# Kernel tuning notes

Measured on AMD Instinct MI355X. Metric: run time of the kernel, lower is better.

## Reference

```python
import jax, jax.numpy as jnp
import numpy as np

LATENT_DIM = 32
NB_LABEL = 10
B = 4096


def _conv4(x, w, b):
    # stride-4 kernel-4 conv == non-overlapping 4x4 patch contraction
    Bn, C, H, W = x.shape
    xp = x.reshape(Bn, C, H // 4, 4, W // 4, 4)
    return jnp.einsum('bcipjq,ocpq->boij', xp, w) + b[None, :, None, None]


def _deconv4(x, w, b):
    # stride-4 kernel-4 ConvTranspose2d, padding 0: each pixel expands to a 4x4 block
    Bn, C, H, W = x.shape
    y = jnp.einsum('bcij,copq->boipjq', x, w)  # w: (Cin, Cout, 4, 4)
    return y.reshape(Bn, w.shape[1], H * 4, W * 4) + b[None, :, None, None]


def setup_inputs() -> dict:
    key = jax.random.key(0)
    ks = jax.random.split(key, 24)
    s = 0.05

    def rn(k, shape, scale=s):
        return jax.random.normal(k, shape, dtype=jnp.float32) * scale

    return {
        'x': jax.random.normal(ks[0], (B, 1, 64, 64), dtype=jnp.float32),
        'z': jax.random.normal(ks[1], (B, NB_LABEL), dtype=jnp.float32),
        'u_in': jax.random.normal(ks[2], (B, 2), dtype=jnp.float32),
        'conv1_w': rn(ks[3], (16, 1, 4, 4)), 'conv1_b': rn(ks[4], (16,)),
        'conv2_w': rn(ks[5], (64, 16, 4, 4)), 'conv2_b': rn(ks[6], (64,)),
        'conv3_w': rn(ks[7], (256, 64, 4, 4)), 'conv3_b': rn(ks[8], (256,)),
        'w_xz': rn(ks[9], (32, 256)),
        'w_label': rn(ks[10], (NB_LABEL, 32)),
        'w_zd1': rn(ks[11], (LATENT_DIM, NB_LABEL)),
        'w_zd2': rn(ks[12], (LATENT_DIM, NB_LABEL)),
        'w_xu': rn(ks[13], (32, 256)),
        'w_mu': rn(ks[14], (2, 32)),
        'w_logvar': rn(ks[15], (2, 32)),
        'tc_w': rn(ks[16], (LATENT_DIM, 256, 2)),
        'tc_b': rn(ks[17], (LATENT_DIM, 256)),
        'dec3_w': rn(ks[18], (256, 64, 4, 4)), 'dec3_b': rn(ks[19], (64,)),
        'dec2_w': rn(ks[20], (64, 16, 4, 4)), 'dec2_b': rn(ks[21], (16,)),
        'dec1_w': rn(ks[22], (16, 1, 4, 4)), 'dec1_b': jnp.zeros((1,), dtype=jnp.float32),
    }


def reference(x, z, u_in, conv1_w, conv1_b, conv2_w, conv2_b, conv3_w, conv3_b,
              w_xz, w_label, w_zd1, w_zd2, w_xu, w_mu, w_logvar, tc_w, tc_b,
              dec3_w, dec3_b, dec2_w, dec2_b, dec1_w, dec1_b):
    h = jax.nn.relu(_conv4(x, conv1_w, conv1_b))
    h = jax.nn.relu(_conv4(h, conv2_w, conv2_b))
    h = jax.nn.relu(_conv4(h, conv3_w, conv3_b))
    h = h.reshape(h.shape[0], -1)                       # (B, 256)

    x_z = jax.nn.relu(h @ w_xz.T)                       # (B, 32)
    z_logit = x_z @ w_label.T                           # (B, 10)

    key = jax.random.key(42)
    k_cat, k_eps = jax.random.split(key)
    z_hat = jax.random.categorical(k_cat, z_logit, axis=-1)       # (B,)
    z_onehot = jax.nn.one_hot(z_hat, NB_LABEL, dtype=z_logit.dtype)
    z_d1 = z_onehot @ w_zd1.T                           # (B, 32)
    z_d2 = z_onehot @ w_zd2.T                           # (B, 32)

    x_u = jax.nn.relu(h @ w_xu.T)                       # (B, 32)
    mu = x_u @ w_mu.T                                   # (B, 2)
    logvar = x_u @ w_logvar.T                           # (B, 2)
    std = jnp.exp(0.5 * logvar)
    eps = jax.random.normal(k_eps, std.shape, dtype=std.dtype)
    u_out = eps * std + mu                              # (B, 2)

    # all 32 tiny Linear(2->256)+ReLU collapsed into one batched einsum
    trans = u_out[:, None, :] + jnp.stack([z_d1, z_d2], axis=-1)   # (B, 32, 2)
    x_hat = jax.nn.relu(jnp.einsum('bic,ioc->bio', trans, tc_w) + tc_b[None]).sum(axis=1)  # (B, 256)
    transfo_d1 = trans[:, :, 0]                         # (B, 32)
    transfo_d2 = trans[:, :, 1]

    d = x_hat.reshape(-1, 256, 1, 1)
    d = jax.nn.relu(_deconv4(d, dec3_w, dec3_b))        # (B, 64, 4, 4)
    d = jax.nn.relu(_deconv4(d, dec2_w, dec2_b))        # (B, 16, 16, 16)
    x_hat_logit = _deconv4(d, dec1_w, dec1_b)           # (B, 1, 64, 64)

    return (z_logit, z_hat.reshape(-1, 1), mu, logvar, u_out, x_hat_logit, transfo_d1, transfo_d2)
```

## Files before the change

### kernel.cpp

```cpp
#include <hip/hip_runtime.h>
#include <stdint.h>

#define B_TOT 4096

#define OFF_ZL 0
#define OFF_ZH 40960
#define OFF_MU 45056
#define OFF_LV 53248
#define OFF_UO 61440
#define OFF_XL 69632
#define OFF_T1 16846848
#define OFF_T2 16977920

typedef __attribute__((ext_vector_type(8))) short bf16x8;
typedef __attribute__((ext_vector_type(4))) float f32x4;

__device__ __forceinline__ unsigned short f2b(float f) {
  unsigned int u = __float_as_uint(f);
  return (unsigned short)((u + 0x7FFFu + ((u >> 16) & 1u)) >> 16);
}
__device__ __forceinline__ float b2f(unsigned short b) {
  return __uint_as_float(((unsigned int)b) << 16);
}

#define TF_ROUND(r) do { x0 += x1; x1 = (x1 << (r)) | (x1 >> (32-(r))); x1 ^= x0; } while(0)

__device__ __forceinline__ void threefry(uint32_t k0, uint32_t k1,
                                         uint32_t c0, uint32_t c1,
                                         uint32_t& o0, uint32_t& o1) {
  uint32_t ks2 = k0 ^ k1 ^ 0x1BD11BDAu;
  uint32_t x0 = c0 + k0, x1 = c1 + k1;
  TF_ROUND(13); TF_ROUND(15); TF_ROUND(26); TF_ROUND(6);
  x0 += k1;  x1 += ks2 + 1u;
  TF_ROUND(17); TF_ROUND(29); TF_ROUND(16); TF_ROUND(24);
  x0 += ks2; x1 += k0 + 2u;
  TF_ROUND(13); TF_ROUND(15); TF_ROUND(26); TF_ROUND(6);
  x0 += k0;  x1 += k1 + 3u;
  TF_ROUND(17); TF_ROUND(29); TF_ROUND(16); TF_ROUND(24);
  x0 += k1;  x1 += ks2 + 4u;
  TF_ROUND(13); TF_ROUND(15); TF_ROUND(26); TF_ROUND(6);
  x0 += ks2; x1 += k0 + 5u;
  o0 = x0; o1 = x1;
}

__device__ __forceinline__ uint32_t tf_bits32(uint32_t k0, uint32_t k1, uint32_t j) {
  uint32_t r0, r1;
  threefry(k0, k1, 0u, j, r0, r1);
  return r0 ^ r1;
}

__device__ __forceinline__ float erfinv_xla(float x) {
  float w = -log1pf(-x * x);
  float p;
  if (w < 5.0f) {
    w -= 2.5f;
    p = 2.81022636e-08f;
    p = fmaf(p, w, 3.43273939e-07f);
    p = fmaf(p, w, -3.5233877e-06f);
    p = fmaf(p, w, -4.39150654e-06f);
    p = fmaf(p, w, 0.00021858087f);
    p = fmaf(p, w, -0.00125372503f);
    p = fmaf(p, w, -0.00417768164f);
    p = fmaf(p, w, 0.246640727f);
    p = fmaf(p, w, 1.50140941f);
  } else {
    w = sqrtf(w) - 3.0f;
    p = -0.000200214257f;
    p = fmaf(p, w, 0.000100950558f);
    p = fmaf(p, w, 0.00134934322f);
    p = fmaf(p, w, -0.00367342844f);
    p = fmaf(p, w, 0.00573950773f);
    p = fmaf(p, w, -0.0076224613f);
    p = fmaf(p, w, 0.00943887047f);
    p = fmaf(p, w, 1.00167406f);
    p = fmaf(p, w, 2.83297682f);
  }
  return p * x;
}

__global__ __launch_bounds__(256) void k_prep(const float* __restrict__ w3,
    const float* __restrict__ w2, unsigned short* __restrict__ w3t,
    unsigned short* __restrict__ w2t) {
  int idx = blockIdx.x * 256 + threadIdx.x;
  unsigned short tmp[8];
  if (idx < 32768) {
    int np = idx >> 5, k0 = (idx & 31) * 8;
    int ic = np & 63, pos = np >> 6;
#pragma unroll
    for (int i = 0; i < 8; ++i)
      tmp[i] = f2b(w3[(size_t)(k0 + i) * 1024 + ic * 16 + pos]);
    *(bf16x8*)(w3t + (size_t)np * 256 + k0) = *(bf16x8*)tmp;
  } else if (idx < 32768 + 2048) {
    int j = idx - 32768;
    int n = j >> 3, k0 = (j & 7) * 8;
#pragma unroll
    for (int i = 0; i < 8; ++i)
      tmp[i] = f2b(w2[(size_t)(k0 + i) * 256 + n]);
    *(bf16x8*)(w2t + (size_t)n * 64 + k0) = *(bf16x8*)tmp;
  }
}

__global__ __launch_bounds__(256) void k_conv1(const float* __restrict__ x,
    const float* __restrict__ w, const float* __restrict__ bias,
    float* __restrict__ h1t) {
  __shared__ __align__(16) float ws[256];
  __shared__ float bs[16];
  int b = blockIdx.x, t = threadIdx.x;
  ws[t] = w[t];
  if (t < 16) bs[t] = bias[t];
  __syncthreads();
  int i = t >> 4, j = t & 15;
  const float* xb = x + (size_t)b * 4096;
  float4 xv[4];
#pragma unroll
  for (int p = 0; p < 4; ++p)
    xv[p] = *(const float4*)(xb + (4 * i + p) * 64 + 4 * j);
  float acc[16];
#pragma unroll
  for (int oc = 0; oc < 16; ++oc) acc[oc] = bs[oc];
#pragma unroll
  for (int p = 0; p < 4; ++p) {
    float4 xp = xv[p];
#pragma unroll
    for (int oc = 0; oc < 16; ++oc) {
      float4 wv = *(const float4*)(ws + oc * 16 + p * 4);
      acc[oc] = fmaf(xp.x, wv.x, acc[oc]);
      acc[oc] = fmaf(xp.y, wv.y, acc[oc]);
      acc[oc] = fmaf(xp.z, wv.z, acc[oc]);
      acc[oc] = fmaf(xp.w, wv.w, acc[oc]);
    }
  }
  float* hb = h1t + (size_t)b * 4096 + ((i >> 2) * 4 + (j >> 2)) * 256
            + (i & 3) * 4 + (j & 3);
#pragma unroll
  for (int oc = 0; oc < 16; ++oc)
    hb[oc * 16] = fmaxf(acc[oc], 0.0f);
}

__global__ __launch_bounds__(256) void k_conv2g(const float* __restrict__ A,
    const float* __restrict__ Bw, const float* __restrict__ bias,
    float* __restrict__ h2) {
  __shared__ __align__(16) float As[16][68];
  __shared__ __align__(16) float Bs[16][68];
  int t = threadIdx.x;
  int m0 = blockIdx.x * 64;
  int tx = t & 15, ty = t >> 4;
  float acc[4][4] = {};
  int lr = t >> 2, lk = (t & 3) * 4;
  for (int k0 = 0; k0 < 256; k0 += 16) {
    float4 a  = *(const float4*)(A  + (size_t)(m0 + lr) * 256 + k0 + lk);
    float4 bv = *(const float4*)(Bw + (size_t)lr * 256 + k0 + lk);
    As[lk + 0][lr] = a.x; As[lk + 1][lr] = a.y; As[lk + 2][lr] = a.z; As[lk + 3][lr] = a.w;
    Bs[lk + 0][lr] = bv.x; Bs[lk + 1][lr] = bv.y; Bs[lk + 2][lr] = bv.z; Bs[lk + 3][lr] = bv.w;
    __syncthreads();
#pragma unroll
    for (int kk = 0; kk < 16; ++kk) {
      float4 af = *(const float4*)(&As[kk][ty * 4]);
      float4 bf = *(const float4*)(&Bs[kk][tx * 4]);
      float av[4] = {af.x, af.y, af.z, af.w};
      float bb[4] = {bf.x, bf.y, bf.z, bf.w};
#pragma unroll
      for (int ii = 0; ii < 4; ++ii)
#pragma unroll
        for (int jj = 0; jj < 4; ++jj)
          acc[ii][jj] = fmaf(av[ii], bb[jj], acc[ii][jj]);
    }
    __syncthreads();
  }
  float4 bb4 = *(const float4*)(bias + tx * 4);
  float bb[4] = {bb4.x, bb4.y, bb4.z, bb4.w};
#pragma unroll
  for (int ii = 0; ii < 4; ++ii) {
    int row = m0 + ty * 4 + ii;
    int b = row >> 4, pos = row & 15;
    float* hp = h2 + (size_t)b * 1024 + pos;
#pragma unroll
    for (int jj = 0; jj < 4; ++jj)
      hp[(tx * 4 + jj) * 16] = fmaxf(acc[ii][jj] + bb[jj], 0.f);
  }
}

__global__ __launch_bounds__(256) void k_conv3p(const float* __restrict__ A,
    const float* __restrict__ w3, float* __restrict__ part) {
  __shared__ __align__(16) float As[16][68];
  __shared__ __align__(16) float Bs[16][68];
  int t = threadIdx.x;
  int m0 = blockIdx.x * 64, n0 = blockIdx.y * 64;
  int kb = blockIdx.z * 256;
  int tx = t & 15, ty = t >> 4;
  float acc[4][4] = {};
  int lr = t >> 2, lk = (t & 3) * 4;
  for (int k0 = kb; k0 < kb + 256; k0 += 16) {
    float4 a  = *(const float4*)(A  + (size_t)(m0 + lr) * 1024 + k0 + lk);
    float4 bv = *(const float4*)(w3 + (size_t)(n0 + lr) * 1024 + k0 + lk);
    As[lk + 0][lr] = a.x; As[lk + 1][lr] = a.y; As[lk + 2][lr] = a.z; As[lk + 3][lr] = a.w;
    Bs[lk + 0][lr] = bv.x; Bs[lk + 1][lr] = bv.y; Bs[lk + 2][lr] = bv.z; Bs[lk + 3][lr] = bv.w;
    __syncthreads();
#pragma unroll
    for (int kk = 0; kk < 16; ++kk) {
      float4 af = *(const float4*)(&As[kk][ty * 4]);
      float4 bf = *(const float4*)(&Bs[kk][tx * 4]);
      float av[4] = {af.x, af.y, af.z, af.w};
      float bb[4] = {bf.x, bf.y, bf.z, bf.w};
#pragma unroll
      for (int ii = 0; ii < 4; ++ii)
#pragma unroll
        for (int jj = 0; jj < 4; ++jj)
          acc[ii][jj] = fmaf(av[ii], bb[jj], acc[ii][jj]);
    }
    __syncthreads();
  }
  float* pc = part + (size_t)blockIdx.z * 1048576;
#pragma unroll
  for (int ii = 0; ii < 4; ++ii) {
    int row = m0 + ty * 4 + ii;
    *(float4*)(pc + (size_t)row * 256 + n0 + tx * 4) =
        make_float4(acc[ii][0], acc[ii][1], acc[ii][2], acc[ii][3]);
  }
}

__global__ __launch_bounds__(256) void k_c3red(const float* __restrict__ part,
    const float* __restrict__ b3, float* __restrict__ h) {
  int idx = blockIdx.x * 256 + threadIdx.x;
  int row = idx >> 6, c4 = (idx & 63) * 4;
  const float* p0 = part + (size_t)row * 256 + c4;
  float4 s  = *(const float4*)(p0);
  float4 s1 = *(const float4*)(p0 + 1048576);
  float4 s2 = *(const float4*)(p0 + 2097152);
  float4 s3 = *(const float4*)(p0 + 3145728);
  float4 bb = *(const float4*)(b3 + c4);
  float4 o;
  o.x = fmaxf(((s.x + s1.x) + s2.x) + s3.x + bb.x, 0.f);
  o.y = fmaxf(((s.y + s1.y) + s2.y) + s3.y + bb.y, 0.f);
  o.z = fmaxf(((s.z + s1.z) + s2.z) + s3.z + bb.z, 0.f);
  o.w = fmaxf(((s.w + s1.w) + s2.w) + s3.w + bb.w, 0.f);
  *(float4*)(h + (size_t)row * 256 + c4) = o;
}

__global__ __launch_bounds__(256) void k_dec3m(const unsigned short* __restrict__ xhb,
    const unsigned short* __restrict__ w3t, const float* __restrict__ bias,
    unsigned short* __restrict__ d3t) {
  int t = threadIdx.x;
  int lane = t & 63, wv = t >> 6;
  int m0 = blockIdx.x * 64, n0 = blockIdx.y * 64;
  int l15 = lane & 15, g8 = (lane >> 4) * 8;
  const unsigned short* arow = xhb + (size_t)(m0 + wv * 16 + l15) * 256 + g8;
  const unsigned short* brow = w3t + (size_t)(n0 + l15) * 256 + g8;
  f32x4 acc[4] = {};
  for (int kb = 0; kb < 256; kb += 32) {
    bf16x8 af = *(const bf16x8*)(arow + kb);
#pragma unroll
    for (int ns = 0; ns < 4; ++ns) {
      bf16x8 bf = *(const bf16x8*)(brow + (size_t)ns * 4096 + kb);
      acc[ns] = __builtin_amdgcn_mfma_f32_16x16x32_bf16(af, bf, acc[ns], 0, 0, 0);
    }
  }
  int rbase = (lane >> 4) * 4;
#pragma unroll
  for (int ns = 0; ns < 4; ++ns) {
    int ncol = n0 + ns * 16 + l15;
    float bb = bias[ncol & 63];
#pragma unroll
    for (int r = 0; r < 4; ++r) {
      float v = fmaxf(acc[ns][r] + bb, 0.f);
      d3t[(size_t)(m0 + wv * 16 + rbase + r) * 1024 + ncol] = f2b(v);
    }
  }
}

__global__ __launch_bounds__(256) void k_dec2m(const unsigned short* __restrict__ d3t,
    const unsigned short* __restrict__ w2t, const float* __restrict__ b2,
    const float* __restrict__ w1, const float* __restrict__ b1,
    float* __restrict__ outp) {
  __shared__ unsigned short d2L[4][4096];
  __shared__ __align__(16) float w1s[256];
  __shared__ float b1s;
  int t = threadIdx.x;
  int lane = t & 63, wv = t >> 6;
  int m0 = blockIdx.x * 64;
  w1s[t] = w1[t];
  if (t == 0) b1s = b1[0];
  int l15 = lane & 15, g8 = (lane >> 4) * 8;
  const unsigned short* arow = d3t + (size_t)(m0 + wv * 16 + l15) * 64 + g8;
  bf16x8 af0 = *(const bf16x8*)(arow);
  bf16x8 af1 = *(const bf16x8*)(arow + 32);
  const unsigned short* brow = w2t + (size_t)l15 * 64 + g8;
  f32x4 acc[16] = {};
#pragma unroll
  for (int ns = 0; ns < 16; ++ns) {
    bf16x8 bf0 = *(const bf16x8*)(brow + (size_t)ns * 1024);
    bf16x8 bf1 = *(const bf16x8*)(brow + (size_t)ns * 1024 + 32);
    acc[ns] = __builtin_amdgcn_mfma_f32_16x16x32_bf16(af0, bf0, acc[ns], 0, 0, 0);
    acc[ns] = __builtin_amdgcn_mfma_f32_16x16x32_bf16(af1, bf1, acc[ns], 0, 0, 0);
  }
  int rbase = (lane >> 4) * 4;
  int pq_p = l15 >> 2, pq_q = l15 & 3;
#pragma unroll
  for (int ns = 0; ns < 16; ++ns) {
    float bb = b2[ns];
#pragma unroll
    for (int r = 0; r < 4; ++r) {
      int pos = rbase + r;
      float v = fmaxf(acc[ns][r] + bb, 0.f);
      d2L[wv][ns * 256 + ((pos >> 2) * 4 + pq_p) * 16 + (pos & 3) * 4 + pq_q] = f2b(v);
    }
  }
  __syncthreads();
  int bg0 = m0 >> 4;
  for (int c4 = 0; c4 < 16; ++c4) {
    int v = t + 256 * c4;
    int bp = v >> 10;
    int I = (v & 1023) >> 4;
    int jpix = v & 15;
    int ipix = I >> 2, pp = I & 3;
    const unsigned short* dl = &d2L[bp][ipix * 16 + jpix];
    float4 o = make_float4(b1s, b1s, b1s, b1s);
#pragma unroll
    for (int c = 0; c < 16; ++c) {
      float dv = b2f(dl[c * 256]);
      float4 wv4 = *(const float4*)(w1s + c * 16 + pp * 4);
      o.x = fmaf(dv, wv4.x, o.x);
      o.y = fmaf(dv, wv4.y, o.y);
      o.z = fmaf(dv, wv4.z, o.z);
      o.w = fmaf(dv, wv4.w, o.w);
    }
    *(float4*)(outp + (size_t)(bg0 + bp) * 4096 + I * 64 + jpix * 4) = o;
  }
}

__global__ __launch_bounds__(256) void k_head(
    const float* __restrict__ h,
    const float* __restrict__ w_xz, const float* __restrict__ w_label,
    const float* __restrict__ w_zd1, const float* __restrict__ w_zd2,
    const float* __restrict__ w_xu, const float* __restrict__ w_mu,
    const float* __restrict__ w_logvar,
    const float* __restrict__ tc_w, const float* __restrict__ tc_b,
    float* __restrict__ outp, unsigned short* __restrict__ xhb) {
  __shared__ __align__(16) float hs[4][256];
  __shared__ float xzs[4][32], xus[4][32];
  __shared__ float zls[4][10], gbs[4][10];
  __shared__ float mus[4][2], lvs[4][2], epss[4][2], uos[4][2];
  __shared__ float t1s[4][32], t2s[4][32];
  __shared__ int zhs[4];
  int t = threadIdx.x;
  int wv = t >> 6, l = t & 63;
  int b = blockIdx.x * 4 + wv;

  *(float4*)(&hs[wv][l * 4]) = *(const float4*)(h + (size_t)b * 256 + l * 4);
  __syncthreads();

  {
    const float* wr = (l < 32) ? (w_xz + l * 256) : (w_xu + (l - 32) * 256);
    float acc = 0.f;
#pragma unroll
    for (int k4 = 0; k4 < 64; ++k4) {
      float4 wvv = *(const float4*)(wr + k4 * 4);
      float4 hv = *(const float4*)(&hs[wv][k4 * 4]);
      acc = fmaf(wvv.x, hv.x, acc);
      acc = fmaf(wvv.y, hv.y, acc);
      acc = fmaf(wvv.z, hv.z, acc);
      acc = fmaf(wvv.w, hv.w, acc);
    }
    acc = fmaxf(acc, 0.f);
    if (l < 32) xzs[wv][l] = acc; else xus[wv][l - 32] = acc;
  }
  __syncthreads();

  if (l < 10) {
    float acc = 0.f;
#pragma unroll
    for (int k = 0; k < 32; ++k) acc = fmaf(xzs[wv][k], w_label[l * 32 + k], acc);
    zls[wv][l] = acc;
    outp[OFF_ZL + (size_t)b * 10 + l] = acc;
  } else if (l < 12) {
    int d = l - 10;
    float acc = 0.f;
#pragma unroll
    for (int k = 0; k < 32; ++k) acc = fmaf(xus[wv][k], w_mu[d * 32 + k], acc);
    mus[wv][d] = acc;
    outp[OFF_MU + (size_t)b * 2 + d] = acc;
  } else if (l < 14) {
    int d = l - 12;
    float acc = 0.f;
#pragma unroll
    for (int k = 0; k < 32; ++k) acc = fmaf(xus[wv][k], w_logvar[d * 32 + k], acc);
    lvs[wv][d] = acc;
    outp[OFF_LV + (size_t)b * 2 + d] = acc;
  }
  __syncthreads();

  if (l < 10) {
    uint32_t kc0, kc1;
    threefry(0u, 42u, 0u, 0u, kc0, kc1);
    uint32_t bits = tf_bits32(kc0, kc1, (uint32_t)(b * 10 + l));
    float f = __uint_as_float((bits >> 9) | 0x3F800000u) - 1.0f;
    float u = fmaxf(f, 1.17549435e-38f);
    float g = -logf(-logf(u));
    gbs[wv][l] = zls[wv][l] + g;
  } else if (l < 12) {
    int d = l - 10;
    uint32_t ke0, ke1;
    threefry(0u, 42u, 0u, 1u, ke0, ke1);
    uint32_t bits = tf_bits32(ke0, ke1, (uint32_t)(b * 2 + d));
    float f = __uint_as_float((bits >> 9) | 0x3F800000u) - 1.0f;
    float u = fmaxf(f * 2.0f - 0.99999994f, -0.99999994f);
    epss[wv][d] = 1.41421356f * erfinv_xla(u);
  }
  __syncthreads();

  if (l == 0) {
    float best = gbs[wv][0];
    int bi = 0;
#pragma unroll
    for (int c = 1; c < 10; ++c) {
      float v = gbs[wv][c];
      if (v > best) { best = v; bi = c; }
    }
    zhs[wv] = bi;
    outp[OFF_ZH + b] = (float)bi;
  } else if (l < 3) {
    int d = l - 1;
    float sd = expf(0.5f * lvs[wv][d]);
    float uo = fmaf(epss[wv][d], sd, mus[wv][d]);
    uos[wv][d] = uo;
    outp[OFF_UO + (size_t)b * 2 + d] = uo;
  }
  __syncthreads();

  if (l < 32) {
    int zh = zhs[wv];
    float t1 = uos[wv][0] + w_zd1[l * 10 + zh];
    float t2 = uos[wv][1] + w_zd2[l * 10 + zh];
    t1s[wv][l] = t1; t2s[wv][l] = t2;
    outp[OFF_T1 + (size_t)b * 32 + l] = t1;
    outp[OFF_T2 + (size_t)b * 32 + l] = t2;
  }
  __syncthreads();

  {
    int o0 = l * 4;
    float4 acc = make_float4(0.f, 0.f, 0.f, 0.f);
#pragma unroll
    for (int i = 0; i < 32; ++i) {
      float t1 = t1s[wv][i], t2 = t2s[wv][i];
      float4 w0 = *(const float4*)(tc_w + ((size_t)i * 256 + o0) * 2);
      float4 w1 = *(const float4*)(tc_w + ((size_t)i * 256 + o0) * 2 + 4);
      float4 tb = *(const float4*)(tc_b + (size_t)i * 256 + o0);
      float s;
      s = fmaf(t1, w0.x, fmaf(t2, w0.y, tb.x)); acc.x += fmaxf(s, 0.f);
      s = fmaf(t1, w0.z, fmaf(t2, w0.w, tb.y)); acc.y += fmaxf(s, 0.f);
      s = fmaf(t1, w1.x, fmaf(t2, w1.y, tb.z)); acc.z += fmaxf(s, 0.f);
      s = fmaf(t1, w1.z, fmaf(t2, w1.w, tb.w)); acc.w += fmaxf(s, 0.f);
    }
    unsigned short pk[4];
    pk[0] = f2b(acc.x); pk[1] = f2b(acc.y); pk[2] = f2b(acc.z); pk[3] = f2b(acc.w);
    *(ushort4*)(xhb + (size_t)b * 256 + o0) = *(ushort4*)pk;
  }
}

extern "C" void kernel_launch(void* const* d_in, const int* in_sizes, int n_in,
                              void* d_out, int out_size, void* d_ws, size_t ws_size,
                              hipStream_t stream) {
  const float* x       = (const float*)d_in[0];
  const float* conv1_w = (const float*)d_in[3];
  const float* conv1_b = (const float*)d_in[4];
  const float* conv2_w = (const float*)d_in[5];
  const float* conv2_b = (const float*)d_in[6];
  const float* conv3_w = (const float*)d_in[7];
  const float* conv3_b = (const float*)d_in[8];
  const float* w_xz    = (const float*)d_in[9];
  const float* w_label = (const float*)d_in[10];
  const float* w_zd1   = (const float*)d_in[11];
  const float* w_zd2   = (const float*)d_in[12];
  const float* w_xu    = (const float*)d_in[13];
  const float* w_mu    = (const float*)d_in[14];
  const float* w_logvar= (const float*)d_in[15];
  const float* tc_w    = (const float*)d_in[16];
  const float* tc_b    = (const float*)d_in[17];
  const float* dec3_w  = (const float*)d_in[18];
  const float* dec3_b  = (const float*)d_in[19];
  const float* dec2_w  = (const float*)d_in[20];
  const float* dec2_b  = (const float*)d_in[21];
  const float* dec1_w  = (const float*)d_in[22];
  const float* dec1_b  = (const float*)d_in[23];

  float* out = (float*)d_out;
  float* ws  = (float*)d_ws;

  float* big = out + OFF_XL;
  float* h2  = ws;
  float* h   = ws + 4194304;
  unsigned short* d3t = (unsigned short*)ws;
  unsigned short* xhb = (unsigned short*)(ws + 5242880);
  unsigned short* w3t = (unsigned short*)(ws + 5767168);
  unsigned short* w2t = (unsigned short*)(ws + 5898240);

  k_prep<<<136, 256, 0, stream>>>(dec3_w, dec2_w, w3t, w2t);
  k_conv1<<<B_TOT, 256, 0, stream>>>(x, conv1_w, conv1_b, big);
  k_conv2g<<<1024, 256, 0, stream>>>(big, conv2_w, conv2_b, h2);
  k_conv3p<<<dim3(64, 4, 4), 256, 0, stream>>>(h2, conv3_w, big);
  k_c3red<<<1024, 256, 0, stream>>>(big, conv3_b, h);
  k_head<<<B_TOT / 4, 256, 0, stream>>>(h, w_xz, w_label, w_zd1, w_zd2, w_xu,
                                        w_mu, w_logvar, tc_w, tc_b, out, xhb);
  k_dec3m<<<dim3(64, 16), 256, 0, stream>>>(xhb, w3t, dec3_b, d3t);
  k_dec2m<<<1024, 256, 0, stream>>>(d3t, w2t, dec2_b, dec1_w, dec1_b, big);
}
```

Baseline: 206.4 us.

## Split head into tiled GEMM kernel and LDS-staged bf16 tail kernel

The first head layer (h @ [w_xz;w_xu]) moves into a separate register-tiled fp32 GEMM kernel. Each 64-row block then reuses its weight tiles instead of every 4-row block re-reading 64KB of weights. The remaining head logic runs in a second kernel that stages tc_w and tc_b into shared memory as bf16 before the per-row transformation sum. This adds a launch, an intermediate buffer, per-block staging of 48KB and bf16 rounding of the transform weights.

```diff
diff --git a/kernel.cpp b/kernel.cpp
--- a/kernel.cpp
+++ b/kernel.cpp
@@ -237,6 +237,173 @@
   *(float4*)(h + (size_t)row * 256 + c4) = o;
 }
 
+__global__ __launch_bounds__(256) void k_headA(const float* __restrict__ A,
+    const float* __restrict__ w_xz, const float* __restrict__ w_xu,
+    float* __restrict__ xzxu) {
+  __shared__ __align__(16) float As[16][68];
+  __shared__ __align__(16) float Bs[16][68];
+  int t = threadIdx.x;
+  int m0 = blockIdx.x * 64;
+  int tx = t & 15, ty = t >> 4;
+  float acc[4][4] = {};
+  int lr = t >> 2, lk = (t & 3) * 4;
+  const float* wr = (lr < 32) ? (w_xz + lr * 256) : (w_xu + (lr - 32) * 256);
+  for (int k0 = 0; k0 < 256; k0 += 16) {
+    float4 a  = *(const float4*)(A + (size_t)(m0 + lr) * 256 + k0 + lk);
+    float4 bv = *(const float4*)(wr + k0 + lk);
+    As[lk + 0][lr] = a.x; As[lk + 1][lr] = a.y; As[lk + 2][lr] = a.z; As[lk + 3][lr] = a.w;
+    Bs[lk + 0][lr] = bv.x; Bs[lk + 1][lr] = bv.y; Bs[lk + 2][lr] = bv.z; Bs[lk + 3][lr] = bv.w;
+    __syncthreads();
+#pragma unroll
+    for (int kk = 0; kk < 16; ++kk) {
+      float4 af = *(const float4*)(&As[kk][ty * 4]);
+      float4 bf = *(const float4*)(&Bs[kk][tx * 4]);
+      float av[4] = {af.x, af.y, af.z, af.w};
+      float bb[4] = {bf.x, bf.y, bf.z, bf.w};
+#pragma unroll
+      for (int ii = 0; ii < 4; ++ii)
+#pragma unroll
+        for (int jj = 0; jj < 4; ++jj)
+          acc[ii][jj] = fmaf(av[ii], bb[jj], acc[ii][jj]);
+    }
+    __syncthreads();
+  }
+#pragma unroll
+  for (int ii = 0; ii < 4; ++ii) {
+    int row = m0 + ty * 4 + ii;
+    float4 o;
+    o.x = fmaxf(acc[ii][0], 0.f);
+    o.y = fmaxf(acc[ii][1], 0.f);
+    o.z = fmaxf(acc[ii][2], 0.f);
+    o.w = fmaxf(acc[ii][3], 0.f);
+    *(float4*)(xzxu + (size_t)row * 64 + tx * 4) = o;
+  }
+}
+
+__global__ __launch_bounds__(256) void k_headB(
+    const float* __restrict__ xzxu,
+    const float* __restrict__ w_label,
+    const float* __restrict__ w_zd1, const float* __restrict__ w_zd2,
+    const float* __restrict__ w_mu, const float* __restrict__ w_logvar,
+    const float* __restrict__ tc_w, const float* __restrict__ tc_b,
+    float* __restrict__ outp, unsigned short* __restrict__ xhb) {
+  __shared__ __align__(16) unsigned short twL[16384];
+  __shared__ __align__(16) unsigned short tbL[8192];
+  __shared__ float xzs[4][32], xus[4][32];
+  __shared__ float zls[4][10], gbs[4][10];
+  __shared__ float mus[4][2], lvs[4][2], epss[4][2], uos[4][2];
+  __shared__ float t1s[4][32], t2s[4][32];
+  __shared__ int zhs[4];
+  int t = threadIdx.x;
+  int wv = t >> 6, l = t & 63;
+  int b = blockIdx.x * 4 + wv;
+
+  for (int v = t; v < 4096; v += 256) {
+    float4 w4 = *(const float4*)(tc_w + (size_t)v * 4);
+    unsigned short pk[4] = {f2b(w4.x), f2b(w4.y), f2b(w4.z), f2b(w4.w)};
+    *(ushort4*)(twL + v * 4) = *(ushort4*)pk;
+  }
+  for (int v = t; v < 2048; v += 256) {
+    float4 b4 = *(const float4*)(tc_b + (size_t)v * 4);
+    unsigned short pk[4] = {f2b(b4.x), f2b(b4.y), f2b(b4.z), f2b(b4.w)};
+    *(ushort4*)(tbL + v * 4) = *(ushort4*)pk;
+  }
+  {
+    float v = xzxu[(size_t)b * 64 + l];
+    if (l < 32) xzs[wv][l] = v; else xus[wv][l - 32] = v;
+  }
+  __syncthreads();
+
+  if (l < 10) {
+    float acc = 0.f;
+#pragma unroll
+    for (int k = 0; k < 32; ++k) acc = fmaf(xzs[wv][k], w_label[l * 32 + k], acc);
+    zls[wv][l] = acc;
+    outp[OFF_ZL + (size_t)b * 10 + l] = acc;
+  } else if (l < 12) {
+    int d = l - 10;
+    float acc = 0.f;
+#pragma unroll
+    for (int k = 0; k < 32; ++k) acc = fmaf(xus[wv][k], w_mu[d * 32 + k], acc);
+    mus[wv][d] = acc;
+    outp[OFF_MU + (size_t)b * 2 + d] = acc;
+  } else if (l < 14) {
+    int d = l - 12;
+    float acc = 0.f;
+#pragma unroll
+    for (int k = 0; k < 32; ++k) acc = fmaf(xus[wv][k], w_logvar[d * 32 + k], acc);
+    lvs[wv][d] = acc;
+    outp[OFF_LV + (size_t)b * 2 + d] = acc;
+  }
+  __syncthreads();
+
+  if (l < 10) {
+    uint32_t kc0, kc1;
+    threefry(0u, 42u, 0u, 0u, kc0, kc1);
+    uint32_t bits = tf_bits32(kc0, kc1, (uint32_t)(b * 10 + l));
+    float f = __uint_as_float((bits >> 9) | 0x3F800000u) - 1.0f;
+    float u = fmaxf(f, 1.17549435e-38f);
+    float g = -logf(-logf(u));
+    gbs[wv][l] = zls[wv][l] + g;
+  } else if (l < 12) {
+    int d = l - 10;
+    uint32_t ke0, ke1;
+    threefry(0u, 42u, 0u, 1u, ke0, ke1);
+    uint32_t bits = tf_bits32(ke0, ke1, (uint32_t)(b * 2 + d));
+    float f = __uint_as_float((bits >> 9) | 0x3F800000u) - 1.0f;
+    float u = fmaxf(f * 2.0f - 0.99999994f, -0.99999994f);
+    epss[wv][d] = 1.41421356f * erfinv_xla(u);
+  }
+  __syncthreads();
+
+  if (l == 0) {
+    float best = gbs[wv][0];
+    int bi = 0;
+#pragma unroll
+    for (int c = 1; c < 10; ++c) {
+      float v = gbs[wv][c];
+      if (v > best) { best = v; bi = c; }
+    }
+    zhs[wv] = bi;
+    outp[OFF_ZH + b] = (float)bi;
+  } else if (l < 3) {
+    int d = l - 1;
+    float sd = expf(0.5f * lvs[wv][d]);
+    float uo = fmaf(epss[wv][d], sd, mus[wv][d]);
+    uos[wv][d] = uo;
+    outp[OFF_UO + (size_t)b * 2 + d] = uo;
+  }
+  __syncthreads();
+
+  if (l < 32) {
+    int zh = zhs[wv];
+    float t1 = uos[wv][0] + w_zd1[l * 10 + zh];
+    float t2 = uos[wv][1] + w_zd2[l * 10 + zh];
+    t1s[wv][l] = t1; t2s[wv][l] = t2;
+    outp[OFF_T1 + (size_t)b * 32 + l] = t1;
+    outp[OFF_T2 + (size_t)b * 32 + l] = t2;
+  }
+  __syncthreads();
+
+  {
+    float ax = 0.f, ay = 0.f, az = 0.f, aw = 0.f;
+#pragma unroll 4
+    for (int i = 0; i < 32; ++i) {
+      float t1 = t1s[wv][i], t2 = t2s[wv][i];
+      ushort4 wa = *(const ushort4*)(twL + i * 512 + l * 8);
+      ushort4 wb = *(const ushort4*)(twL + i * 512 + l * 8 + 4);
+      ushort4 tb = *(const ushort4*)(tbL + i * 256 + l * 4);
+      float s;
+      s = fmaf(t1, b2f(wa.x), fmaf(t2, b2f(wa.y), b2f(tb.x))); ax += fmaxf(s, 0.f);
+      s = fmaf(t1, b2f(wa.z), fmaf(t2, b2f(wa.w), b2f(tb.y))); ay += fmaxf(s, 0.f);
+      s = fmaf(t1, b2f(wb.x), fmaf(t2, b2f(wb.y), b2f(tb.z))); az += fmaxf(s, 0.f);
+      s = fmaf(t1, b2f(wb.z), fmaf(t2, b2f(wb.w), b2f(tb.w))); aw += fmaxf(s, 0.f);
+    }
+    unsigned short pk[4] = {f2b(ax), f2b(ay), f2b(az), f2b(aw)};
+    *(ushort4*)(xhb + (size_t)b * 256 + l * 4) = *(ushort4*)pk;
+  }
+}
+
 __global__ __launch_bounds__(256) void k_dec3m(const unsigned short* __restrict__ xhb,
     const unsigned short* __restrict__ w3t, const float* __restrict__ bias,
     unsigned short* __restrict__ d3t) {
@@ -325,136 +492,6 @@
       o.w = fmaf(dv, wv4.w, o.w);
     }
     *(float4*)(outp + (size_t)(bg0 + bp) * 4096 + I * 64 + jpix * 4) = o;
-  }
-}
-
-__global__ __launch_bounds__(256) void k_head(
-    const float* __restrict__ h,
-    const float* __restrict__ w_xz, const float* __restrict__ w_label,
-    const float* __restrict__ w_zd1, const float* __restrict__ w_zd2,
-    const float* __restrict__ w_xu, const float* __restrict__ w_mu,
-    const float* __restrict__ w_logvar,
-    const float* __restrict__ tc_w, const float* __restrict__ tc_b,
-    float* __restrict__ outp, unsigned short* __restrict__ xhb) {
-  __shared__ __align__(16) float hs[4][256];
-  __shared__ float xzs[4][32], xus[4][32];
-  __shared__ float zls[4][10], gbs[4][10];
-  __shared__ float mus[4][2], lvs[4][2], epss[4][2], uos[4][2];
-  __shared__ float t1s[4][32], t2s[4][32];
-  __shared__ int zhs[4];
-  int t = threadIdx.x;
-  int wv = t >> 6, l = t & 63;
-  int b = blockIdx.x * 4 + wv;
-
-  *(float4*)(&hs[wv][l * 4]) = *(const float4*)(h + (size_t)b * 256 + l * 4);
-  __syncthreads();
-
-  {
-    const float* wr = (l < 32) ? (w_xz + l * 256) : (w_xu + (l - 32) * 256);
-    float acc = 0.f;
-#pragma unroll
-    for (int k4 = 0; k4 < 64; ++k4) {
-      float4 wvv = *(const float4*)(wr + k4 * 4);
-      float4 hv = *(const float4*)(&hs[wv][k4 * 4]);
-      acc = fmaf(wvv.x, hv.x, acc);
-      acc = fmaf(wvv.y, hv.y, acc);
-      acc = fmaf(wvv.z, hv.z, acc);
-      acc = fmaf(wvv.w, hv.w, acc);
-    }
-    acc = fmaxf(acc, 0.f);
-    if (l < 32) xzs[wv][l] = acc; else xus[wv][l - 32] = acc;
-  }
-  __syncthreads();
-
-  if (l < 10) {
-    float acc = 0.f;
-#pragma unroll
-    for (int k = 0; k < 32; ++k) acc = fmaf(xzs[wv][k], w_label[l * 32 + k], acc);
-    zls[wv][l] = acc;
-    outp[OFF_ZL + (size_t)b * 10 + l] = acc;
-  } else if (l < 12) {
-    int d = l - 10;
-    float acc = 0.f;
-#pragma unroll
-    for (int k = 0; k < 32; ++k) acc = fmaf(xus[wv][k], w_mu[d * 32 + k], acc);
-    mus[wv][d] = acc;
-    outp[OFF_MU + (size_t)b * 2 + d] = acc;
-  } else if (l < 14) {
-    int d = l - 12;
-    float acc = 0.f;
-#pragma unroll
-    for (int k = 0; k < 32; ++k) acc = fmaf(xus[wv][k], w_logvar[d * 32 + k], acc);
-    lvs[wv][d] = acc;
-    outp[OFF_LV + (size_t)b * 2 + d] = acc;
-  }
-  __syncthreads();
-
-  if (l < 10) {
-    uint32_t kc0, kc1;
-    threefry(0u, 42u, 0u, 0u, kc0, kc1);
-    uint32_t bits = tf_bits32(kc0, kc1, (uint32_t)(b * 10 + l));
-    float f = __uint_as_float((bits >> 9) | 0x3F800000u) - 1.0f;
-    float u = fmaxf(f, 1.17549435e-38f);
-    float g = -logf(-logf(u));
-    gbs[wv][l] = zls[wv][l] + g;
-  } else if (l < 12) {
-    int d = l - 10;
-    uint32_t ke0, ke1;
-    threefry(0u, 42u, 0u, 1u, ke0, ke1);
-    uint32_t bits = tf_bits32(ke0, ke1, (uint32_t)(b * 2 + d));
-    float f = __uint_as_float((bits >> 9) | 0x3F800000u) - 1.0f;
-    float u = fmaxf(f * 2.0f - 0.99999994f, -0.99999994f);
-    epss[wv][d] = 1.41421356f * erfinv_xla(u);
-  }
-  __syncthreads();
-
-  if (l == 0) {
-    float best = gbs[wv][0];
-    int bi = 0;
-#pragma unroll
-    for (int c = 1; c < 10; ++c) {
-      float v = gbs[wv][c];
-      if (v > best) { best = v; bi = c; }
-    }
-    zhs[wv] = bi;
-    outp[OFF_ZH + b] = (float)bi;
-  } else if (l < 3) {
-    int d = l - 1;
-    float sd = expf(0.5f * lvs[wv][d]);
-    float uo = fmaf(epss[wv][d], sd, mus[wv][d]);
-    uos[wv][d] = uo;
-    outp[OFF_UO + (size_t)b * 2 + d] = uo;
-  }
-  __syncthreads();
-
-  if (l < 32) {
-    int zh = zhs[wv];
-    float t1 = uos[wv][0] + w_zd1[l * 10 + zh];
-    float t2 = uos[wv][1] + w_zd2[l * 10 + zh];
-    t1s[wv][l] = t1; t2s[wv][l] = t2;
-    outp[OFF_T1 + (size_t)b * 32 + l] = t1;
-    outp[OFF_T2 + (size_t)b * 32 + l] = t2;
-  }
-  __syncthreads();
-
-  {
-    int o0 = l * 4;
-    float4 acc = make_float4(0.f, 0.f, 0.f, 0.f);
-#pragma unroll
-    for (int i = 0; i < 32; ++i) {
-      float t1 = t1s[wv][i], t2 = t2s[wv][i];
-      float4 w0 = *(const float4*)(tc_w + ((size_t)i * 256 + o0) * 2);
-      float4 w1 = *(const float4*)(tc_w + ((size_t)i * 256 + o0) * 2 + 4);
-      float4 tb = *(const float4*)(tc_b + (size_t)i * 256 + o0);
-      float s;
-      s = fmaf(t1, w0.x, fmaf(t2, w0.y, tb.x)); acc.x += fmaxf(s, 0.f);
-      s = fmaf(t1, w0.z, fmaf(t2, w0.w, tb.y)); acc.y += fmaxf(s, 0.f);
-      s = fmaf(t1, w1.x, fmaf(t2, w1.y, tb.z)); acc.z += fmaxf(s, 0.f);
-      s = fmaf(t1, w1.z, fmaf(t2, w1.w, tb.w)); acc.w += fmaxf(s, 0.f);
-    }
-    unsigned short pk[4];
-    pk[0] = f2b(acc.x); pk[1] = f2b(acc.y); pk[2] = f2b(acc.z); pk[3] = f2b(acc.w);
-    *(ushort4*)(xhb + (size_t)b * 256 + o0) = *(ushort4*)pk;
   }
 }
 
@@ -494,14 +531,16 @@
   unsigned short* xhb = (unsigned short*)(ws + 5242880);
   unsigned short* w3t = (unsigned short*)(ws + 5767168);
   unsigned short* w2t = (unsigned short*)(ws + 5898240);
+  float* xzxu = ws + 5906432;
 
   k_prep<<<136, 256, 0, stream>>>(dec3_w, dec2_w, w3t, w2t);
   k_conv1<<<B_TOT, 256, 0, stream>>>(x, conv1_w, conv1_b, big);
   k_conv2g<<<1024, 256, 0, stream>>>(big, conv2_w, conv2_b, h2);
   k_conv3p<<<dim3(64, 4, 4), 256, 0, stream>>>(h2, conv3_w, big);
   k_c3red<<<1024, 256, 0, stream>>>(big, conv3_b, h);
-  k_head<<<B_TOT / 4, 256, 0, stream>>>(h, w_xz, w_label, w_zd1, w_zd2, w_xu,
-                                        w_mu, w_logvar, tc_w, tc_b, out, xhb);
+  k_headA<<<64, 256, 0, stream>>>(h, w_xz, w_xu, xzxu);
+  k_headB<<<B_TOT / 4, 256, 0, stream>>>(xzxu, w_label, w_zd1, w_zd2, w_mu,
+                                         w_logvar, tc_w, tc_b, out, xhb);
   k_dec3m<<<dim3(64, 16), 256, 0, stream>>>(xhb, w3t, dec3_b, d3t);
   k_dec2m<<<1024, 256, 0, stream>>>(d3t, w2t, dec2_b, dec1_w, dec1_b, big);
 }
```

Result: faster. 194.7 us (-5.7%).
